# Performance work log

Measured on AMD Instinct MI355X. Metric: run time of the kernel, lower is better.

Reference implementation:

```python
import jax, jax.numpy as jnp
import numpy as np

T, N, E = 8, 20000, 320000
F_IN, HID, HEADS, GH = 32, 64, 4, 128


def setup_inputs() -> dict:
    key = jax.random.key(0)
    ks = jax.random.split(key, 20)
    rn = lambda k, s, sc=0.05: jax.random.normal(k, s, jnp.float32) * sc
    return {
        "x_seq": jax.random.normal(ks[0], (T, N, F_IN), jnp.float32),
        "edge_index": jax.random.randint(ks[1], (2, E), 0, N),
        # GATConv 1: in=F_IN, out=HID, heads=HEADS, concat=True
        "W1": rn(ks[2], (F_IN, HEADS * HID)),
        "a_src1": rn(ks[3], (HEADS, HID)),
        "a_dst1": rn(ks[4], (HEADS, HID)),
        "b1": jnp.zeros((HEADS * HID,), jnp.float32),
        # GATConv 2: in=HEADS*HID, out=HID, heads=1, concat=False
        "W2": rn(ks[5], (HEADS * HID, HID)),
        "a_src2": rn(ks[6], (1, HID)),
        "a_dst2": rn(ks[7], (1, HID)),
        "b2": jnp.zeros((HID,), jnp.float32),
        # GRU layer 0 (input 2*HID) and layer 1 (input GH); torch gate order r,z,n
        "Wih0": rn(ks[8], (3 * GH, 2 * HID)),
        "Whh0": rn(ks[9], (3 * GH, GH)),
        "bih0": jnp.zeros((3 * GH,), jnp.float32),
        "bhh0": jnp.zeros((3 * GH,), jnp.float32),
        "Wih1": rn(ks[10], (3 * GH, GH)),
        "Whh1": rn(ks[11], (3 * GH, GH)),
        "bih1": jnp.zeros((3 * GH,), jnp.float32),
        "bhh1": jnp.zeros((3 * GH,), jnp.float32),
        # decoder MLP
        "Wd1": rn(ks[12], (GH, GH // 2)),
        "bd1": jnp.zeros((GH // 2,), jnp.float32),
        "Wd2": rn(ks[13], (GH // 2, 1)),
        "bd2": jnp.zeros((1,), jnp.float32),
    }


def _gat(x, W, a_s, a_d, b, src, dst, heads, out_ch, concat):
    """PyG-style GATConv with self-loops already included in (src, dst)."""
    n = x.shape[0]
    h = (x @ W).reshape(n, heads, out_ch)            # [N, H, C]
    al_s = (h * a_s).sum(-1)                          # [N, H]
    al_d = (h * a_d).sum(-1)
    e = jax.nn.leaky_relu(al_s[src] + al_d[dst], 0.2)  # [Etot, H]
    m = jax.ops.segment_max(e, dst, num_segments=n)
    ex = jnp.exp(e - m[dst])
    s = jax.ops.segment_sum(ex, dst, num_segments=n)
    att = ex / (s[dst] + 1e-16)
    out = jax.ops.segment_sum(h[src] * att[..., None], dst, num_segments=n)
    out = out.reshape(n, heads * out_ch) if concat else out.mean(axis=1)
    return out + b


def _gru_layer(xs, Wih, Whh, bih, bhh):
    # xs: [T, B, D]; torch GRU cell, gate order r,z,n
    def step(hp, x):
        gi = x @ Wih.T + bih
        gh = hp @ Whh.T + bhh
        ir, iz, inn = jnp.split(gi, 3, axis=-1)
        hr, hz, hn = jnp.split(gh, 3, axis=-1)
        r = jax.nn.sigmoid(ir + hr)
        z = jax.nn.sigmoid(iz + hz)
        nn_ = jnp.tanh(inn + r * hn)
        h = (1.0 - z) * nn_ + z * hp
        return h, h
    h0 = jnp.zeros((xs.shape[1], Whh.shape[1]), xs.dtype)
    hT, ys = jax.lax.scan(step, h0, xs)
    return hT, ys


def reference(x_seq, edge_index, W1, a_src1, a_dst1, b1, W2, a_src2, a_dst2, b2,
              Wih0, Whh0, bih0, bhh0, Wih1, Whh1, bih1, bhh1, Wd1, bd1, Wd2, bd2):
    n = x_seq.shape[1]
    loops = jnp.arange(n)
    src = jnp.concatenate([edge_index[0], loops])
    dst = jnp.concatenate([edge_index[1], loops])

    def encode(x):                                    # x: [N, F_IN]
        h = jax.nn.elu(_gat(x, W1, a_src1, a_dst1, b1, src, dst, HEADS, HID, True))
        h = _gat(h, W2, a_src2, a_dst2, b2, src, dst, 1, HID, False)
        return jnp.concatenate([h[edge_index[0]], h[edge_index[1]]], axis=-1)  # [E, 2*HID]

    emb = jax.vmap(encode)(x_seq)                     # [T, E, 2*HID]
    _, ys0 = _gru_layer(emb, Wih0, Whh0, bih0, bhh0)
    hT1, _ = _gru_layer(ys0, Wih1, Whh1, bih1, bhh1)  # last-layer final hidden [E, GH]
    pred = jax.nn.relu(hT1 @ Wd1 + bd1) @ Wd2 + bd2   # [E, 1]
    return pred
```

## Files before the change

### kernel.cpp

```cpp
#include <hip/hip_runtime.h>
#include <hip/hip_fp16.h>
#include <math.h>

#define T_ 8
#define N_ 20000
#define E_ 320000
#define ETOT_ (E_ + N_)
#define FIN_ 32
#define C1_ 256
#define HID_ 64
#define G3_ 384
#define GH_ 128
#define MB_ 64
#define MT_ 4
#define LDP_ 136
#define SEG_ 2
#define ESEG_ (E_ / SEG_)
#define NPACK_ (24 * 4 * 64 * 8)

typedef __attribute__((ext_vector_type(8))) _Float16 h8v;
typedef __attribute__((ext_vector_type(4))) float f4v;

__device__ __forceinline__ float wave_sum(float v) {
#pragma unroll
  for (int off = 32; off; off >>= 1) v += __shfl_down(v, off);
  return v;
}
__device__ __forceinline__ float sigmoidf_(float x) { return 1.f / (1.f + __expf(-x)); }
__device__ __forceinline__ float tanhf_(float x) {
  float e2 = __expf(2.f * x);
  return 1.f - 2.f / (e2 + 1.f);
}
__device__ __forceinline__ unsigned short f2h(float f) {
  return __half_as_ushort(__float2half_rn(f));
}
__device__ __forceinline__ float h2f(unsigned short u) {
  return __half2float(__ushort_as_half(u));
}
__device__ __forceinline__ void edge_sd(const int* ei, int e, int& s, int& d) {
  if (e < E_) { s = ei[e]; d = ei[E_ + e]; }
  else { s = e - E_; d = e - E_; }
}

__global__ void k_hist(const int* __restrict__ ei, int* __restrict__ counts) {
  int e = blockIdx.x * 256 + threadIdx.x;
  if (e >= ETOT_) return;
  int s, d; edge_sd(ei, e, s, d);
  atomicAdd(&counts[d], 1);
}

__global__ void k_scan(const int* __restrict__ counts, int* __restrict__ indptr) {
  __shared__ int tmp[1024];
  __shared__ int carry;
  int tid = threadIdx.x;
  if (tid == 0) { carry = 0; indptr[0] = 0; }
  __syncthreads();
  for (int base = 0; base < N_; base += 1024) {
    int i = base + tid;
    int v = (i < N_) ? counts[i] : 0;
    tmp[tid] = v;
    __syncthreads();
    for (int off = 1; off < 1024; off <<= 1) {
      int add = (tid >= off) ? tmp[tid - off] : 0;
      __syncthreads();
      tmp[tid] += add;
      __syncthreads();
    }
    if (i < N_) indptr[i + 1] = carry + tmp[tid];
    __syncthreads();
    if (tid == 1023) carry += tmp[1023];
    __syncthreads();
  }
}

__global__ void k_copy(const int* __restrict__ indptr, int* __restrict__ cursors) {
  int i = blockIdx.x * 256 + threadIdx.x;
  if (i < N_) cursors[i] = indptr[i];
}

__global__ void k_scatter(const int* __restrict__ ei, int* __restrict__ cursors,
                          int* __restrict__ csr_src) {
  int e = blockIdx.x * 256 + threadIdx.x;
  if (e >= ETOT_) return;
  int s, d; edge_sd(ei, e, s, d);
  int pos = atomicAdd(&cursors[d], 1);
  csr_src[pos] = s;
}

__global__ void k_packW16(const float* __restrict__ W, unsigned short* __restrict__ Bh) {
  int idx = blockIdx.x * 256 + threadIdx.x;
  if (idx >= NPACK_) return;
  int j = idx & 7, lane = (idx >> 3) & 63, ks = (idx >> 9) & 3, nt = idx >> 11;
  int n = nt * 16 + (lane & 15);
  int k = ks * 32 + (lane >> 4) * 8 + j;
  Bh[idx] = f2h(W[n * GH_ + k]);
}

__global__ __launch_bounds__(256) void k_gat1_lin(
    const float* __restrict__ x, const float* __restrict__ W1,
    const float* __restrict__ as1, const float* __restrict__ ad1,
    unsigned short* __restrict__ hlin, float* __restrict__ als, float* __restrict__ ald) {
  int n = blockIdx.x;
  int j = threadIdx.x;
  __shared__ float sx[FIN_];
  if (j < FIN_) sx[j] = x[n * FIN_ + j];
  __syncthreads();
  float acc = 0.f;
#pragma unroll
  for (int k = 0; k < FIN_; ++k) acc = fmaf(sx[k], W1[k * C1_ + j], acc);
  hlin[(size_t)n * C1_ + j] = f2h(acc);
  int h = j >> 6, c = j & 63;
  float vs = wave_sum(acc * as1[h * 64 + c]);
  float vd = wave_sum(acc * ad1[h * 64 + c]);
  if (c == 0) { als[n * 4 + h] = vs; ald[n * 4 + h] = vd; }
}

__global__ __launch_bounds__(256) void k_gat1_attn(
    const int* __restrict__ csr_src, const int* __restrict__ indptr,
    const float* __restrict__ als, const float* __restrict__ ald,
    float* __restrict__ ex, float* __restrict__ sums) {
  int w = threadIdx.x >> 6, lane = threadIdx.x & 63;
  int n = blockIdx.x * 4 + w;
  int s0 = indptr[n], s1 = indptr[n + 1];
  float adv[4], mx[4], sm[4];
#pragma unroll
  for (int h = 0; h < 4; ++h) { adv[h] = ald[n * 4 + h]; mx[h] = -1e30f; sm[h] = 0.f; }
  for (int e = s0 + lane; e < s1; e += 64) {
    int s = csr_src[e];
#pragma unroll
    for (int h = 0; h < 4; ++h) {
      float sc = als[s * 4 + h] + adv[h];
      sc = sc >= 0.f ? sc : 0.2f * sc;
      ex[(size_t)e * 4 + h] = sc;
      mx[h] = fmaxf(mx[h], sc);
    }
  }
#pragma unroll
  for (int h = 0; h < 4; ++h) {
#pragma unroll
    for (int off = 32; off; off >>= 1) mx[h] = fmaxf(mx[h], __shfl_xor(mx[h], off));
  }
  for (int e = s0 + lane; e < s1; e += 64) {
#pragma unroll
    for (int h = 0; h < 4; ++h) {
      float v = __expf(ex[(size_t)e * 4 + h] - mx[h]);
      ex[(size_t)e * 4 + h] = v;
      sm[h] += v;
    }
  }
#pragma unroll
  for (int h = 0; h < 4; ++h) sm[h] = wave_sum(sm[h]);
  if (lane == 0) {
#pragma unroll
    for (int h = 0; h < 4; ++h) sums[n * 4 + h] = sm[h];
  }
}

__global__ __launch_bounds__(256) void k_gat1_agg(
    const int* __restrict__ csr_src, const int* __restrict__ indptr,
    const float* __restrict__ ex, const float* __restrict__ sums,
    const unsigned short* __restrict__ hlin, const float* __restrict__ b1,
    float* __restrict__ h1out) {
  int n = blockIdx.x;
  int j = threadIdx.x;
  int hh = j >> 6;
  int s0 = indptr[n], s1 = indptr[n + 1];
  float inv = 1.f / (sums[n * 4 + hh] + 1e-16f);
  float acc = 0.f;
  for (int e = s0; e < s1; ++e) {
    int s = csr_src[e];
    float a = ex[(size_t)e * 4 + hh] * inv;
    acc = fmaf(a, h2f(hlin[(size_t)s * C1_ + j]), acc);
  }
  float o = acc + b1[j];
  h1out[(size_t)n * C1_ + j] = o > 0.f ? o : expm1f(o);
}

__global__ __launch_bounds__(256) void k_gat2_lin(
    const float* __restrict__ h1out, const float* __restrict__ W2,
    const float* __restrict__ as2, const float* __restrict__ ad2,
    unsigned short* __restrict__ hlin2, float* __restrict__ als, float* __restrict__ ald) {
  int w = threadIdx.x >> 6, lane = threadIdx.x & 63;
  int n = blockIdx.x * 4 + w;
  __shared__ float sx[4][C1_];
  for (int k = lane; k < C1_; k += 64) sx[w][k] = h1out[(size_t)n * C1_ + k];
  __syncthreads();
  float acc = 0.f;
#pragma unroll 4
  for (int k = 0; k < C1_; ++k) acc = fmaf(sx[w][k], W2[k * HID_ + lane], acc);
  hlin2[(size_t)n * HID_ + lane] = f2h(acc);
  float vs = wave_sum(acc * as2[lane]);
  float vd = wave_sum(acc * ad2[lane]);
  if (lane == 0) { als[n] = vs; ald[n] = vd; }
}

__global__ __launch_bounds__(256) void k_gat2_attn(
    const int* __restrict__ csr_src, const int* __restrict__ indptr,
    const float* __restrict__ als, const float* __restrict__ ald,
    float* __restrict__ ex, float* __restrict__ sums) {
  int w = threadIdx.x >> 6, lane = threadIdx.x & 63;
  int n = blockIdx.x * 4 + w;
  int s0 = indptr[n], s1 = indptr[n + 1];
  float adv = ald[n];
  float mx = -1e30f, sm = 0.f;
  for (int e = s0 + lane; e < s1; e += 64) {
    float sc = als[csr_src[e]] + adv;
    sc = sc >= 0.f ? sc : 0.2f * sc;
    ex[e] = sc;
    mx = fmaxf(mx, sc);
  }
#pragma unroll
  for (int off = 32; off; off >>= 1) mx = fmaxf(mx, __shfl_xor(mx, off));
  for (int e = s0 + lane; e < s1; e += 64) {
    float v = __expf(ex[e] - mx);
    ex[e] = v;
    sm += v;
  }
  sm = wave_sum(sm);
  if (lane == 0) sums[n] = sm;
}

__global__ __launch_bounds__(256) void k_gat2_agg(
    const int* __restrict__ csr_src, const int* __restrict__ indptr,
    const float* __restrict__ ex, const float* __restrict__ sums,
    const unsigned short* __restrict__ hlin2, const float* __restrict__ b2,
    unsigned short* __restrict__ h2f16) {
  int w = threadIdx.x >> 6, lane = threadIdx.x & 63;
  int n = blockIdx.x * 4 + w;
  int s0 = indptr[n], s1 = indptr[n + 1];
  float inv = 1.f / (sums[n] + 1e-16f);
  float acc = 0.f;
  for (int e = s0; e < s1; ++e) {
    int s = csr_src[e];
    acc = fmaf(ex[e] * inv, h2f(hlin2[(size_t)s * HID_ + lane]), acc);
  }
  h2f16[(size_t)n * HID_ + lane] = f2h(acc + b2[lane]);
}

__device__ __forceinline__ void mfma1h(f4v& acc, h8v a, h8v b) {
  acc = __builtin_amdgcn_mfma_f32_16x16x32_f16(a, b, acc, 0, 0, 0);
}

__device__ __forceinline__ void mfma_pass(
    const unsigned short* A_,
    const unsigned short* __restrict__ Bh_,
    int w, int lane, f4v Cr[MT_], f4v Cz[MT_], f4v Cn[MT_]) {
  const int mrow = lane & 15, quad = lane >> 4;
#pragma unroll
  for (int ks = 0; ks < 4; ++ks) {
    h8v A[MT_];
    const int aoff = mrow * LDP_ + ks * 32 + quad * 8;
#pragma unroll
    for (int mt = 0; mt < MT_; ++mt) A[mt] = *(const h8v*)(A_ + aoff + mt * (16 * LDP_));
    {
      const int nt = w;
      const h8v bh = *(const h8v*)(Bh_ + ((size_t)(nt * 4 + ks) * 64 + lane) * 8);
#pragma unroll
      for (int mt = 0; mt < MT_; ++mt) mfma1h(Cr[mt], A[mt], bh);
    }
    {
      const int nt = 8 + w;
      const h8v bh = *(const h8v*)(Bh_ + ((size_t)(nt * 4 + ks) * 64 + lane) * 8);
#pragma unroll
      for (int mt = 0; mt < MT_; ++mt) mfma1h(Cz[mt], A[mt], bh);
    }
    {
      const int nt = 16 + w;
      const h8v bh = *(const h8v*)(Bh_ + ((size_t)(nt * 4 + ks) * 64 + lane) * 8);
#pragma unroll
      for (int mt = 0; mt < MT_; ++mt) mfma1h(Cn[mt], A[mt], bh);
    }
  }
}

__device__ __forceinline__ void mfma_pass_x(
    const unsigned short* __restrict__ h2,
    const int esrc[MT_], const int edst[MT_],
    const unsigned short* __restrict__ Bh_,
    int w, int lane, f4v Cr[MT_], f4v Cz[MT_], f4v Cn[MT_]) {
  const int quad = lane >> 4;
#pragma unroll
  for (int ks = 0; ks < 4; ++ks) {
    h8v A[MT_];
    const int choff = (ks & 1) * 32 + quad * 8;
#pragma unroll
    for (int mt = 0; mt < MT_; ++mt) {
      const int node = (ks < 2) ? esrc[mt] : edst[mt];
      A[mt] = *(const h8v*)(h2 + (size_t)node * HID_ + choff);
    }
    {
      const int nt = w;
      const h8v bh = *(const h8v*)(Bh_ + ((size_t)(nt * 4 + ks) * 64 + lane) * 8);
#pragma unroll
      for (int mt = 0; mt < MT_; ++mt) mfma1h(Cr[mt], A[mt], bh);
    }
    {
      const int nt = 8 + w;
      const h8v bh = *(const h8v*)(Bh_ + ((size_t)(nt * 4 + ks) * 64 + lane) * 8);
#pragma unroll
      for (int mt = 0; mt < MT_; ++mt) mfma1h(Cz[mt], A[mt], bh);
    }
    {
      const int nt = 16 + w;
      const h8v bh = *(const h8v*)(Bh_ + ((size_t)(nt * 4 + ks) * 64 + lane) * 8);
#pragma unroll
      for (int mt = 0; mt < MT_; ++mt) mfma1h(Cn[mt], A[mt], bh);
    }
  }
}

__global__ __launch_bounds__(512, 4) void k_gru_step(
    const unsigned short* __restrict__ h2, const int* __restrict__ ei,
    int seg_e0, int first, int last,
    const unsigned short* __restrict__ pWih0, const unsigned short* __restrict__ pWhh0,
    const unsigned short* __restrict__ pWih1, const unsigned short* __restrict__ pWhh1,
    const float* __restrict__ bih0, const float* __restrict__ bhh0,
    const float* __restrict__ bih1, const float* __restrict__ bhh1,
    const float* __restrict__ Wd1, const float* __restrict__ bd1,
    const float* __restrict__ Wd2, const float* __restrict__ bd2,
    unsigned short* __restrict__ h0g, unsigned short* __restrict__ h1g,
    float* __restrict__ out) {
  __shared__ unsigned short h0h[MB_ * LDP_];
  __shared__ unsigned short h1h[MB_ * LDP_];
  const int tid = threadIdx.x;
  const int lane = tid & 63, w = tid >> 6;
  const int col = lane & 15, quad = lane >> 4;
  const int mrow = lane & 15;
  const int le0 = blockIdx.x * MB_;
  const size_t ge0 = (size_t)seg_e0 + le0;

  if (!first) {
    for (int i = tid; i < MB_ * 16; i += 512) {
      int e = i >> 4, c = (i & 15) * 8;
      *(h8v*)&h0h[e * LDP_ + c] =
          __builtin_nontemporal_load((const h8v*)(h0g + (size_t)(le0 + e) * GH_ + c));
      *(h8v*)&h1h[e * LDP_ + c] =
          __builtin_nontemporal_load((const h8v*)(h1g + (size_t)(le0 + e) * GH_ + c));
    }
  }
  int esrc[MT_], edst[MT_];
#pragma unroll
  for (int mt = 0; mt < MT_; ++mt) {
    esrc[mt] = ei[ge0 + mt * 16 + mrow];
    edst[mt] = ei[E_ + ge0 + mt * 16 + mrow];
  }
  __syncthreads();

  const int cg = w * 16 + col;
  f4v Cr[MT_], Cz[MT_], Cin[MT_], Chn[MT_];

#pragma unroll
  for (int mt = 0; mt < MT_; ++mt) {
    Cr[mt] = (f4v){0.f, 0.f, 0.f, 0.f};
    Cz[mt] = (f4v){0.f, 0.f, 0.f, 0.f};
    Cin[mt] = (f4v){0.f, 0.f, 0.f, 0.f};
    Chn[mt] = (f4v){0.f, 0.f, 0.f, 0.f};
  }
  mfma_pass_x(h2, esrc, edst, pWih0, w, lane, Cr, Cz, Cin);
  if (!first) mfma_pass(h0h, pWhh0, w, lane, Cr, Cz, Chn);
  __syncthreads();
  {
    float biR = bih0[cg] + bhh0[cg];
    float biZ = bih0[128 + cg] + bhh0[128 + cg];
    float biNi = bih0[256 + cg], biNh = bhh0[256 + cg];
#pragma unroll
    for (int mt = 0; mt < MT_; ++mt)
#pragma unroll
      for (int reg = 0; reg < 4; ++reg) {
        int e = mt * 16 + quad * 4 + reg;
        float r = sigmoidf_(Cr[mt][reg] + biR);
        float z = sigmoidf_(Cz[mt][reg] + biZ);
        float n = tanhf_(Cin[mt][reg] + biNi + r * (Chn[mt][reg] + biNh));
        float hp = first ? 0.f : h2f(h0h[e * LDP_ + cg]);
        float hv = (1.f - z) * n + z * hp;
        h0h[e * LDP_ + cg] = f2h(hv);
      }
  }
  __syncthreads();

#pragma unroll
  for (int mt = 0; mt < MT_; ++mt) {
    Cr[mt] = (f4v){0.f, 0.f, 0.f, 0.f};
    Cz[mt] = (f4v){0.f, 0.f, 0.f, 0.f};
    Cin[mt] = (f4v){0.f, 0.f, 0.f, 0.f};
    Chn[mt] = (f4v){0.f, 0.f, 0.f, 0.f};
  }
  mfma_pass(h0h, pWih1, w, lane, Cr, Cz, Cin);
  if (!first) mfma_pass(h1h, pWhh1, w, lane, Cr, Cz, Chn);
  __syncthreads();
  {
    float biR = bih1[cg] + bhh1[cg];
    float biZ = bih1[128 + cg] + bhh1[128 + cg];
    float biNi = bih1[256 + cg], biNh = bhh1[256 + cg];
#pragma unroll
    for (int mt = 0; mt < MT_; ++mt)
#pragma unroll
      for (int reg = 0; reg < 4; ++reg) {
        int e = mt * 16 + quad * 4 + reg;
        float r = sigmoidf_(Cr[mt][reg] + biR);
        float z = sigmoidf_(Cz[mt][reg] + biZ);
        float n = tanhf_(Cin[mt][reg] + biNi + r * (Chn[mt][reg] + biNh));
        float hp = first ? 0.f : h2f(h1h[e * LDP_ + cg]);
        float hv = (1.f - z) * n + z * hp;
        if (!last) {
          h1h[e * LDP_ + cg] = f2h(hv);
        } else {
          unsigned short hb = f2h(hv);
          h1h[e * LDP_ + cg] = hb;
          h0h[e * LDP_ + cg] = f2h(hv - h2f(hb));
        }
      }
  }
  __syncthreads();

  if (!last) {
    for (int i = tid; i < MB_ * 16; i += 512) {
      int e = i >> 4, c = (i & 15) * 8;
      __builtin_nontemporal_store(*(const h8v*)&h0h[e * LDP_ + c],
                                  (h8v*)(h0g + (size_t)(le0 + e) * GH_ + c));
      __builtin_nontemporal_store(*(const h8v*)&h1h[e * LDP_ + c],
                                  (h8v*)(h1g + (size_t)(le0 + e) * GH_ + c));
    }
  } else {
    for (int ee = 0; ee < MB_ / 8; ++ee) {
      int e = w * (MB_ / 8) + ee;
      float acc = 0.f;
#pragma unroll
      for (int kc = 0; kc < 16; ++kc) {
        h8v hv8 = *(const h8v*)&h1h[e * LDP_ + kc * 8];
        h8v lv8 = *(const h8v*)&h0h[e * LDP_ + kc * 8];
#pragma unroll
        for (int j = 0; j < 8; ++j) {
          float hvv = (float)hv8[j] + (float)lv8[j];
          acc = fmaf(hvv, Wd1[(kc * 8 + j) * 64 + lane], acc);
        }
      }
      float rv = fmaxf(acc + bd1[lane], 0.f);
      float contrib = wave_sum(rv * Wd2[lane]);
      if (lane == 0) out[ge0 + e] = contrib + bd2[0];
    }
  }
}

extern "C" void kernel_launch(void* const* d_in, const int* in_sizes, int n_in,
                              void* d_out, int out_size, void* d_ws, size_t ws_size,
                              hipStream_t stream) {
  (void)in_sizes; (void)n_in; (void)out_size; (void)ws_size;
  const float* x_seq = (const float*)d_in[0];
  const int*   ei    = (const int*)d_in[1];
  const float* W1    = (const float*)d_in[2];
  const float* as1   = (const float*)d_in[3];
  const float* ad1   = (const float*)d_in[4];
  const float* b1    = (const float*)d_in[5];
  const float* W2    = (const float*)d_in[6];
  const float* as2   = (const float*)d_in[7];
  const float* ad2   = (const float*)d_in[8];
  const float* b2    = (const float*)d_in[9];
  const float* Wih0  = (const float*)d_in[10];
  const float* Whh0  = (const float*)d_in[11];
  const float* bih0  = (const float*)d_in[12];
  const float* bhh0  = (const float*)d_in[13];
  const float* Wih1  = (const float*)d_in[14];
  const float* Whh1  = (const float*)d_in[15];
  const float* bih1  = (const float*)d_in[16];
  const float* bhh1  = (const float*)d_in[17];
  const float* Wd1   = (const float*)d_in[18];
  const float* bd1   = (const float*)d_in[19];
  const float* Wd2   = (const float*)d_in[20];
  const float* bd2   = (const float*)d_in[21];
  float* out = (float*)d_out;

  char* p = (char*)d_ws;
  auto alloc = [&](size_t bytes) -> char* {
    char* r = p;
    p += (bytes + 255) & ~(size_t)255;
    return r;
  };
  unsigned short* h2_all = (unsigned short*)alloc((size_t)T_ * N_ * HID_ * 2);
  unsigned short* pWih0 = (unsigned short*)alloc(NPACK_ * 2);
  unsigned short* pWhh0 = (unsigned short*)alloc(NPACK_ * 2);
  unsigned short* pWih1 = (unsigned short*)alloc(NPACK_ * 2);
  unsigned short* pWhh1 = (unsigned short*)alloc(NPACK_ * 2);
  int* counts   = (int*)alloc((size_t)N_ * 4);
  int* indptr   = (int*)alloc((size_t)(N_ + 1) * 4);
  int* cursors  = (int*)alloc((size_t)N_ * 4);
  int* csr      = (int*)alloc((size_t)ETOT_ * 4);
  char* region = p;
  unsigned short* hlin1 = (unsigned short*)(region);
  char* q = region + (((size_t)N_ * C1_ * 2 + 255) & ~(size_t)255);
  float* h1out  = (float*)q; q += ((size_t)N_ * C1_ * 4 + 255) & ~(size_t)255;
  unsigned short* hlin2 = (unsigned short*)q; q += ((size_t)N_ * HID_ * 2 + 255) & ~(size_t)255;
  float* als1   = (float*)q; q += ((size_t)N_ * 16 + 255) & ~(size_t)255;
  float* ald1   = (float*)q; q += ((size_t)N_ * 16 + 255) & ~(size_t)255;
  float* sums1  = (float*)q; q += ((size_t)N_ * 16 + 255) & ~(size_t)255;
  float* als2   = (float*)q; q += ((size_t)N_ * 4 + 255) & ~(size_t)255;
  float* ald2   = (float*)q; q += ((size_t)N_ * 4 + 255) & ~(size_t)255;
  float* sums2  = (float*)q; q += ((size_t)N_ * 4 + 255) & ~(size_t)255;
  float* ex1    = (float*)q; q += ((size_t)ETOT_ * 16 + 255) & ~(size_t)255;
  float* ex2    = (float*)q; q += ((size_t)ETOT_ * 4 + 255) & ~(size_t)255;
  unsigned short* h0g = (unsigned short*)(region);
  unsigned short* h1g = (unsigned short*)(region + (((size_t)ESEG_ * GH_ * 2 + 255) & ~(size_t)255));

  (void)hipMemsetAsync(counts, 0, (size_t)N_ * 4, stream);

  k_hist<<<(ETOT_ + 255) / 256, 256, 0, stream>>>(ei, counts);
  k_scan<<<1, 1024, 0, stream>>>(counts, indptr);
  k_copy<<<(N_ + 255) / 256, 256, 0, stream>>>(indptr, cursors);
  k_scatter<<<(ETOT_ + 255) / 256, 256, 0, stream>>>(ei, cursors, csr);
  const int pb = (NPACK_ + 255) / 256;
  k_packW16<<<pb, 256, 0, stream>>>(Wih0, pWih0);
  k_packW16<<<pb, 256, 0, stream>>>(Whh0, pWhh0);
  k_packW16<<<pb, 256, 0, stream>>>(Wih1, pWih1);
  k_packW16<<<pb, 256, 0, stream>>>(Whh1, pWhh1);

  for (int t = 0; t < T_; ++t) {
    const float* xt = x_seq + (size_t)t * N_ * FIN_;
    unsigned short* h2t = h2_all + (size_t)t * N_ * HID_;
    k_gat1_lin<<<N_, 256, 0, stream>>>(xt, W1, as1, ad1, hlin1, als1, ald1);
    k_gat1_attn<<<N_ / 4, 256, 0, stream>>>(csr, indptr, als1, ald1, ex1, sums1);
    k_gat1_agg<<<N_, 256, 0, stream>>>(csr, indptr, ex1, sums1, hlin1, b1, h1out);
    k_gat2_lin<<<N_ / 4, 256, 0, stream>>>(h1out, W2, as2, ad2, hlin2, als2, ald2);
    k_gat2_attn<<<N_ / 4, 256, 0, stream>>>(csr, indptr, als2, ald2, ex2, sums2);
    k_gat2_agg<<<N_ / 4, 256, 0, stream>>>(csr, indptr, ex2, sums2, hlin2, b2, h2t);
  }

  for (int seg = 0; seg < SEG_; ++seg) {
    for (int t = 0; t < T_; ++t) {
      const unsigned short* h2t = h2_all + (size_t)t * N_ * HID_;
      k_gru_step<<<ESEG_ / MB_, 512, 0, stream>>>(
          h2t, ei, seg * ESEG_, (t == 0) ? 1 : 0, (t == T_ - 1) ? 1 : 0,
          pWih0, pWhh0, pWih1, pWhh1,
          bih0, bhh0, bih1, bhh1, Wd1, bd1, Wd2, bd2,
          h0g, h1g, out);
    }
  }
}
```

Baseline: 4.895 ms.

## Batch GAT kernels over timesteps and fuse layer-1 aggregation with layer-2 linear

The GAT encoder kernels now take a grid y-dimension over the timesteps with per-timestep strides, so all timesteps run in one launch each when the workspace is large enough. The layer-1 aggregation kernel is merged with the layer-2 linear projection: the ELU output stays in shared memory and four waves each compute a partial K-slice that is summed at the end, which removes the h1out global round trip. Larger grids are meant to improve occupancy and cut launch count, at the cost of a workspace about T times larger, with the old per-timestep loop kept as a fallback.

```diff
diff --git a/kernel.cpp b/kernel.cpp
--- a/kernel.cpp
+++ b/kernel.cpp
@@ -97,9 +97,12 @@
 }
 
 __global__ __launch_bounds__(256) void k_gat1_lin(
-    const float* __restrict__ x, const float* __restrict__ W1,
+    const float* __restrict__ x, size_t xs, const float* __restrict__ W1,
     const float* __restrict__ as1, const float* __restrict__ ad1,
-    unsigned short* __restrict__ hlin, float* __restrict__ als, float* __restrict__ ald) {
+    unsigned short* __restrict__ hlin, size_t hs,
+    float* __restrict__ als, float* __restrict__ ald, size_t avs) {
+  size_t t = blockIdx.y;
+  x += t * xs; hlin += t * hs; als += t * avs; ald += t * avs;
   int n = blockIdx.x;
   int j = threadIdx.x;
   __shared__ float sx[FIN_];
@@ -117,8 +120,10 @@
 
 __global__ __launch_bounds__(256) void k_gat1_attn(
     const int* __restrict__ csr_src, const int* __restrict__ indptr,
-    const float* __restrict__ als, const float* __restrict__ ald,
-    float* __restrict__ ex, float* __restrict__ sums) {
+    const float* __restrict__ als, const float* __restrict__ ald, size_t avs,
+    float* __restrict__ ex, size_t exs, float* __restrict__ sums, size_t ss) {
+  size_t t = blockIdx.y;
+  als += t * avs; ald += t * avs; ex += t * exs; sums += t * ss;
   int w = threadIdx.x >> 6, lane = threadIdx.x & 63;
   int n = blockIdx.x * 4 + w;
   int s0 = indptr[n], s1 = indptr[n + 1];
@@ -156,48 +161,55 @@
   }
 }
 
-__global__ __launch_bounds__(256) void k_gat1_agg(
+__global__ __launch_bounds__(256) void k_agg1lin2(
     const int* __restrict__ csr_src, const int* __restrict__ indptr,
-    const float* __restrict__ ex, const float* __restrict__ sums,
-    const unsigned short* __restrict__ hlin, const float* __restrict__ b1,
-    float* __restrict__ h1out) {
+    const float* __restrict__ ex, size_t exs, const float* __restrict__ sums, size_t ss,
+    const unsigned short* __restrict__ hlin, size_t hs, const float* __restrict__ b1,
+    const float* __restrict__ W2, const float* __restrict__ as2, const float* __restrict__ ad2,
+    unsigned short* __restrict__ hlin2, size_t h2s,
+    float* __restrict__ als2, float* __restrict__ ald2, size_t a2s) {
+  size_t t = blockIdx.y;
+  ex += t * exs; sums += t * ss; hlin += t * hs;
+  hlin2 += t * h2s; als2 += t * a2s; ald2 += t * a2s;
   int n = blockIdx.x;
   int j = threadIdx.x;
-  int hh = j >> 6;
+  int w = j >> 6, lane = j & 63;
+  __shared__ float sh1[C1_];
+  __shared__ float part[4][68];
   int s0 = indptr[n], s1 = indptr[n + 1];
-  float inv = 1.f / (sums[n * 4 + hh] + 1e-16f);
+  float inv = 1.f / (sums[n * 4 + w] + 1e-16f);
   float acc = 0.f;
   for (int e = s0; e < s1; ++e) {
     int s = csr_src[e];
-    float a = ex[(size_t)e * 4 + hh] * inv;
+    float a = ex[(size_t)e * 4 + w] * inv;
     acc = fmaf(a, h2f(hlin[(size_t)s * C1_ + j]), acc);
   }
   float o = acc + b1[j];
-  h1out[(size_t)n * C1_ + j] = o > 0.f ? o : expm1f(o);
-}
-
-__global__ __launch_bounds__(256) void k_gat2_lin(
-    const float* __restrict__ h1out, const float* __restrict__ W2,
-    const float* __restrict__ as2, const float* __restrict__ ad2,
-    unsigned short* __restrict__ hlin2, float* __restrict__ als, float* __restrict__ ald) {
-  int w = threadIdx.x >> 6, lane = threadIdx.x & 63;
-  int n = blockIdx.x * 4 + w;
-  __shared__ float sx[4][C1_];
-  for (int k = lane; k < C1_; k += 64) sx[w][k] = h1out[(size_t)n * C1_ + k];
-  __syncthreads();
-  float acc = 0.f;
+  sh1[j] = o > 0.f ? o : expm1f(o);
+  __syncthreads();
+  float pw = 0.f;
 #pragma unroll 4
-  for (int k = 0; k < C1_; ++k) acc = fmaf(sx[w][k], W2[k * HID_ + lane], acc);
-  hlin2[(size_t)n * HID_ + lane] = f2h(acc);
-  float vs = wave_sum(acc * as2[lane]);
-  float vd = wave_sum(acc * ad2[lane]);
-  if (lane == 0) { als[n] = vs; ald[n] = vd; }
+  for (int kk = 0; kk < 64; ++kk) {
+    int k = w * 64 + kk;
+    pw = fmaf(sh1[k], W2[k * HID_ + lane], pw);
+  }
+  part[w][lane] = pw;
+  __syncthreads();
+  if (w == 0) {
+    float a2 = part[0][lane] + part[1][lane] + part[2][lane] + part[3][lane];
+    hlin2[(size_t)n * HID_ + lane] = f2h(a2);
+    float vs = wave_sum(a2 * as2[lane]);
+    float vd = wave_sum(a2 * ad2[lane]);
+    if (lane == 0) { als2[n] = vs; ald2[n] = vd; }
+  }
 }
 
 __global__ __launch_bounds__(256) void k_gat2_attn(
     const int* __restrict__ csr_src, const int* __restrict__ indptr,
-    const float* __restrict__ als, const float* __restrict__ ald,
-    float* __restrict__ ex, float* __restrict__ sums) {
+    const float* __restrict__ als, const float* __restrict__ ald, size_t a2s,
+    float* __restrict__ ex, size_t e2s, float* __restrict__ sums, size_t s2s) {
+  size_t t = blockIdx.y;
+  als += t * a2s; ald += t * a2s; ex += t * e2s; sums += t * s2s;
   int w = threadIdx.x >> 6, lane = threadIdx.x & 63;
   int n = blockIdx.x * 4 + w;
   int s0 = indptr[n], s1 = indptr[n + 1];
@@ -222,9 +234,11 @@
 
 __global__ __launch_bounds__(256) void k_gat2_agg(
     const int* __restrict__ csr_src, const int* __restrict__ indptr,
-    const float* __restrict__ ex, const float* __restrict__ sums,
-    const unsigned short* __restrict__ hlin2, const float* __restrict__ b2,
-    unsigned short* __restrict__ h2f16) {
+    const float* __restrict__ ex, size_t e2s, const float* __restrict__ sums, size_t s2s,
+    const unsigned short* __restrict__ hlin2, size_t h2s, const float* __restrict__ b2,
+    unsigned short* __restrict__ h2f16, size_t hos) {
+  size_t t = blockIdx.y;
+  ex += t * e2s; sums += t * s2s; hlin2 += t * h2s; h2f16 += t * hos;
   int w = threadIdx.x >> 6, lane = threadIdx.x & 63;
   int n = blockIdx.x * 4 + w;
   int s0 = indptr[n], s1 = indptr[n + 1];
@@ -445,7 +459,7 @@
 extern "C" void kernel_launch(void* const* d_in, const int* in_sizes, int n_in,
                               void* d_out, int out_size, void* d_ws, size_t ws_size,
                               hipStream_t stream) {
-  (void)in_sizes; (void)n_in; (void)out_size; (void)ws_size;
+  (void)in_sizes; (void)n_in; (void)out_size;
   const float* x_seq = (const float*)d_in[0];
   const int*   ei    = (const int*)d_in[1];
   const float* W1    = (const float*)d_in[2];
@@ -476,6 +490,8 @@
     p += (bytes + 255) & ~(size_t)255;
     return r;
   };
+  auto rnd = [](size_t b) { return (b + 255) & ~(size_t)255; };
+
   unsigned short* h2_all = (unsigned short*)alloc((size_t)T_ * N_ * HID_ * 2);
   unsigned short* pWih0 = (unsigned short*)alloc(NPACK_ * 2);
   unsigned short* pWhh0 = (unsigned short*)alloc(NPACK_ * 2);
@@ -485,21 +501,35 @@
   int* indptr   = (int*)alloc((size_t)(N_ + 1) * 4);
   int* cursors  = (int*)alloc((size_t)N_ * 4);
   int* csr      = (int*)alloc((size_t)ETOT_ * 4);
+
+  const size_t S_HL1 = (size_t)N_ * C1_;
+  const size_t S_EX1 = (size_t)ETOT_ * 4;
+  const size_t S_SU1 = (size_t)N_ * 4;
+  const size_t S_HL2 = (size_t)N_ * HID_;
+  const size_t S_EX2 = (size_t)ETOT_;
+  const size_t S_SC2 = (size_t)N_;
+
+  size_t gat_batched = rnd(S_HL1 * 2 * T_) + rnd(S_EX1 * 4 * T_) + 3 * rnd(S_SU1 * 4 * T_) +
+                       rnd(S_HL2 * 2 * T_) + rnd(S_EX2 * 4 * T_) + 3 * rnd(S_SC2 * 4 * T_);
+  size_t states_b = 2 * rnd((size_t)ESEG_ * GH_ * 2);
+  size_t pers_off = (size_t)(p - (char*)d_ws);
+  size_t region_need = gat_batched > states_b ? gat_batched : states_b;
+  const int batched = (ws_size >= pers_off + region_need + (1u << 20)) ? 1 : 0;
+  const size_t TB = batched ? T_ : 1;
+
   char* region = p;
-  unsigned short* hlin1 = (unsigned short*)(region);
-  char* q = region + (((size_t)N_ * C1_ * 2 + 255) & ~(size_t)255);
-  float* h1out  = (float*)q; q += ((size_t)N_ * C1_ * 4 + 255) & ~(size_t)255;
-  unsigned short* hlin2 = (unsigned short*)q; q += ((size_t)N_ * HID_ * 2 + 255) & ~(size_t)255;
-  float* als1   = (float*)q; q += ((size_t)N_ * 16 + 255) & ~(size_t)255;
-  float* ald1   = (float*)q; q += ((size_t)N_ * 16 + 255) & ~(size_t)255;
-  float* sums1  = (float*)q; q += ((size_t)N_ * 16 + 255) & ~(size_t)255;
-  float* als2   = (float*)q; q += ((size_t)N_ * 4 + 255) & ~(size_t)255;
-  float* ald2   = (float*)q; q += ((size_t)N_ * 4 + 255) & ~(size_t)255;
-  float* sums2  = (float*)q; q += ((size_t)N_ * 4 + 255) & ~(size_t)255;
-  float* ex1    = (float*)q; q += ((size_t)ETOT_ * 16 + 255) & ~(size_t)255;
-  float* ex2    = (float*)q; q += ((size_t)ETOT_ * 4 + 255) & ~(size_t)255;
+  unsigned short* hlin1 = (unsigned short*)alloc(S_HL1 * 2 * TB);
+  float* ex1    = (float*)alloc(S_EX1 * 4 * TB);
+  float* als1   = (float*)alloc(S_SU1 * 4 * TB);
+  float* ald1   = (float*)alloc(S_SU1 * 4 * TB);
+  float* sums1  = (float*)alloc(S_SU1 * 4 * TB);
+  unsigned short* hlin2 = (unsigned short*)alloc(S_HL2 * 2 * TB);
+  float* ex2    = (float*)alloc(S_EX2 * 4 * TB);
+  float* als2   = (float*)alloc(S_SC2 * 4 * TB);
+  float* ald2   = (float*)alloc(S_SC2 * 4 * TB);
+  float* sums2  = (float*)alloc(S_SC2 * 4 * TB);
   unsigned short* h0g = (unsigned short*)(region);
-  unsigned short* h1g = (unsigned short*)(region + (((size_t)ESEG_ * GH_ * 2 + 255) & ~(size_t)255));
+  unsigned short* h1g = (unsigned short*)(region + rnd((size_t)ESEG_ * GH_ * 2));
 
   (void)hipMemsetAsync(counts, 0, (size_t)N_ * 4, stream);
 
@@ -513,15 +543,22 @@
   k_packW16<<<pb, 256, 0, stream>>>(Wih1, pWih1);
   k_packW16<<<pb, 256, 0, stream>>>(Whh1, pWhh1);
 
-  for (int t = 0; t < T_; ++t) {
-    const float* xt = x_seq + (size_t)t * N_ * FIN_;
-    unsigned short* h2t = h2_all + (size_t)t * N_ * HID_;
-    k_gat1_lin<<<N_, 256, 0, stream>>>(xt, W1, as1, ad1, hlin1, als1, ald1);
-    k_gat1_attn<<<N_ / 4, 256, 0, stream>>>(csr, indptr, als1, ald1, ex1, sums1);
-    k_gat1_agg<<<N_, 256, 0, stream>>>(csr, indptr, ex1, sums1, hlin1, b1, h1out);
-    k_gat2_lin<<<N_ / 4, 256, 0, stream>>>(h1out, W2, as2, ad2, hlin2, als2, ald2);
-    k_gat2_attn<<<N_ / 4, 256, 0, stream>>>(csr, indptr, als2, ald2, ex2, sums2);
-    k_gat2_agg<<<N_ / 4, 256, 0, stream>>>(csr, indptr, ex2, sums2, hlin2, b2, h2t);
+  const int TL = batched ? 1 : T_;
+  const unsigned gy = batched ? T_ : 1;
+  for (int t = 0; t < TL; ++t) {
+    const float* xt = batched ? x_seq : x_seq + (size_t)t * N_ * FIN_;
+    unsigned short* h2t = batched ? h2_all : h2_all + (size_t)t * N_ * HID_;
+    k_gat1_lin<<<dim3(N_, gy), 256, 0, stream>>>(
+        xt, (size_t)N_ * FIN_, W1, as1, ad1, hlin1, S_HL1, als1, ald1, S_SU1);
+    k_gat1_attn<<<dim3(N_ / 4, gy), 256, 0, stream>>>(
+        csr, indptr, als1, ald1, S_SU1, ex1, S_EX1, sums1, S_SU1);
+    k_agg1lin2<<<dim3(N_, gy), 256, 0, stream>>>(
+        csr, indptr, ex1, S_EX1, sums1, S_SU1, hlin1, S_HL1, b1,
+        W2, as2, ad2, hlin2, S_HL2, als2, ald2, S_SC2);
+    k_gat2_attn<<<dim3(N_ / 4, gy), 256, 0, stream>>>(
+        csr, indptr, als2, ald2, S_SC2, ex2, S_EX2, sums2, S_SC2);
+    k_gat2_agg<<<dim3(N_ / 4, gy), 256, 0, stream>>>(
+        csr, indptr, ex2, S_EX2, sums2, S_SC2, hlin2, S_HL2, b2, h2t, S_HL2);
   }
 
   for (int seg = 0; seg < SEG_; ++seg) {
```

Measured after the change: 4.646 ms. 5.1% less time.
